# Kernel tuning notes

Measured on AMD Instinct MI355X. Metric: run time of the kernel, lower is better.

Reference implementation:

```python
import jax, jax.numpy as jnp
import numpy as np
from jax import lax

D = 768
C = 37          # num_classes + 1
PAD_ID = C - 1  # label_init puts '[PAD]' last
B, S = 128, 512


def setup_inputs() -> dict:
    key = jax.random.key(0)
    ks = jax.random.split(key, 8)
    x = jax.random.normal(ks[0], (B, S, D), dtype=jnp.float32)
    W = jax.random.normal(ks[1], (D, C), dtype=jnp.float32) * (1.0 / np.sqrt(D))
    b = jnp.zeros((C,), dtype=jnp.float32)
    start = jax.random.uniform(ks[2], (C,), minval=-0.1, maxval=0.1)
    end = jax.random.uniform(ks[3], (C,), minval=-0.1, maxval=0.1)
    trans = jax.random.uniform(ks[4], (C, C), minval=-0.1, maxval=0.1)
    labels = jax.random.randint(ks[5], (B, S), 0, C)
    lengths = jax.random.randint(ks[6], (B,), 16, S + 1)
    mask = (jnp.arange(S)[None, :] < lengths[:, None])  # first column always True
    return {"x": x, "W": W, "b": b, "start": start, "end": end,
            "trans": trans, "labels": labels, "mask": mask}


def _crf(emissions, labels, mask, start, end, trans):
    # time-major, as in pytorch-crf
    em = jnp.transpose(emissions, (1, 0, 2))      # [S, B, C]
    tg = labels.T                                  # [S, B]
    mkb = mask.T                                   # [S, B] bool
    mkf = mkb.astype(em.dtype)
    bidx = jnp.arange(em.shape[1])

    # ---- gold path score ----
    score0 = start[tg[0]] + em[0, bidx, tg[0]]
    def step_score(carry, inp):
        prev_tag, s = carry
        e_t, t_t, mf, mb = inp
        s = s + (trans[prev_tag, t_t] + e_t[bidx, t_t]) * mf
        prev_tag = jnp.where(mb, t_t, prev_tag)
        return (prev_tag, s), None
    (last_tag, score), _ = lax.scan(step_score, (tg[0], score0),
                                    (em[1:], tg[1:], mkf[1:], mkb[1:]))
    score = score + end[last_tag]

    # ---- log partition (forward algorithm) ----
    alpha0 = start[None, :] + em[0]               # [B, C]
    def step_norm(alpha, inp):
        e_t, mb = inp
        nxt = jax.nn.logsumexp(alpha[:, :, None] + trans[None, :, :], axis=1) + e_t
        return jnp.where(mb[:, None], nxt, alpha), None
    alpha, _ = lax.scan(step_norm, alpha0, (em[1:], mkb[1:]))
    logZ = jax.nn.logsumexp(alpha + end[None, :], axis=1)
    ll = jnp.sum(score - logZ)                    # reduction='sum'

    # ---- Viterbi decode ----
    ident = jnp.arange(C)[None, :]
    v0 = start[None, :] + em[0]
    def step_vit(v, inp):
        e_t, mb = inp
        cand = v[:, :, None] + trans[None, :, :]  # [B, prev, cur]
        bp = jnp.argmax(cand, axis=1)             # [B, C]
        nxt = jnp.max(cand, axis=1) + e_t
        v = jnp.where(mb[:, None], nxt, v)
        bp = jnp.where(mb[:, None], bp, ident)    # identity at padded steps
        return v, bp
    v, bps = lax.scan(step_vit, v0, (em[1:], mkb[1:]))  # bps: [S-1, B, C]
    last = jnp.argmax(v + end[None, :], axis=1)   # [B]
    def back(tag, bp):
        return bp[bidx, tag], tag
    first, rest = lax.scan(back, last, bps, reverse=True)
    tags = jnp.concatenate([first[None, :], rest], axis=0).T  # [B, S]
    tags = jnp.where(mask, tags, PAD_ID)
    return ll, tags


def reference(x, W, b, start, end, trans, labels, mask):
    emissions = jnp.einsum('bsd,dc->bsc', x, W) + b  # linear head
    log_likelihood, tags = _crf(emissions, labels, mask, start, end, trans)
    return log_likelihood, tags
```

## Files before the change

### kernel.cpp

```cpp
#include <hip/hip_runtime.h>

#define Bq 128
#define Sq 512
#define Cq 37
#define Dq 768
#define VST 40

typedef __attribute__((ext_vector_type(2))) float f32x2;
typedef __attribute__((ext_vector_type(4))) float f32x4;
typedef __attribute__((ext_vector_type(8))) short bf16x8;

static __device__ __forceinline__ f32x2 pk_fma(f32x2 a, f32x2 b, f32x2 c) {
  f32x2 d; asm("v_pk_fma_f32 %0, %1, %2, %3" : "=v"(d) : "v"(a), "v"(b), "v"(c));
  return d;
}
static __device__ __forceinline__ f32x2 pk_add(f32x2 a, f32x2 b) {
  f32x2 d; asm("v_pk_add_f32 %0, %1, %2" : "=v"(d) : "v"(a), "v"(b));
  return d;
}
static __device__ __forceinline__ float bcast(float v, int p) {
  return __int_as_float(__builtin_amdgcn_ds_bpermute(p << 2, __float_as_int(v)));
}

#define REP18(X) X(0)X(1)X(2)X(3)X(4)X(5)X(6)X(7)X(8)X(9)X(10)X(11)X(12)X(13) \
  X(14)X(15)X(16)X(17)
#define REP37(X) X(0)X(1)X(2)X(3)X(4)X(5)X(6)X(7)X(8)X(9)X(10)X(11)X(12)X(13) \
  X(14)X(15)X(16)X(17)X(18)X(19)X(20)X(21)X(22)X(23)X(24)X(25)X(26)X(27)X(28) \
  X(29)X(30)X(31)X(32)X(33)X(34)X(35)X(36)

__global__ __launch_bounds__(256) void prep_kernel(
    const float* __restrict__ W, unsigned short* __restrict__ Wbh,
    unsigned short* __restrict__ Wbl)
{
  int i = blockIdx.x * 256 + threadIdx.x;
  if (i >= 24 * 3 * 64 * 8) return;
  int ks = i / 1536, rem = i % 1536;
  int nt = rem / 512, rem2 = rem % 512;
  int lane = rem2 >> 3, j = rem2 & 7;
  int k = ks * 32 + (lane >> 4) * 8 + j;
  int c = nt * 16 + (lane & 15);
  float w = (c < Cq) ? W[(size_t)k * Cq + c] : 0.f;
  unsigned u = __float_as_uint(w);
  unsigned short h = (unsigned short)(u >> 16);
  float hr = __uint_as_float((unsigned)h << 16);
  float r = w - hr;
  Wbh[i] = h;
  Wbl[i] = (unsigned short)(__float_as_uint(r) >> 16);
}

__global__ __launch_bounds__(256) void emis_kernel(
    const float* __restrict__ x, const unsigned short* __restrict__ Wbh,
    const unsigned short* __restrict__ Wbl, const float* __restrict__ bias,
    float* __restrict__ em)
{
  int tid = threadIdx.x, lane = tid & 63;
  int wv = tid >> 6;
  int tokBase = blockIdx.x * 64 + wv * 16;
  int row = lane & 15, kg = lane >> 4;
  const float* xr = x + (size_t)(tokBase + row) * Dq + kg * 8;
  const bf16x8* Bh = (const bf16x8*)Wbh;
  const bf16x8* Bl = (const bf16x8*)Wbl;
  f32x4 acc0 = {0.f, 0.f, 0.f, 0.f};
  f32x4 acc1 = {0.f, 0.f, 0.f, 0.f};
  f32x4 acc2 = {0.f, 0.f, 0.f, 0.f};

  float4 c0 = *(const float4*)(xr);
  float4 c1 = *(const float4*)(xr + 4);
  for (int ks = 0; ks < 24; ++ks) {
    float4 n0, n1;
    if (ks < 23) {
      n0 = *(const float4*)(xr + (ks + 1) * 32);
      n1 = *(const float4*)(xr + (ks + 1) * 32 + 4);
    }
    bf16x8 ah, al;
#define SPLIT(J, V) { unsigned u = __float_as_uint(V); \
    unsigned short h = (unsigned short)(u >> 16); \
    float hr = __uint_as_float((unsigned)h << 16); \
    float rr = (V) - hr; \
    ah[J] = (short)h; al[J] = (short)(__float_as_uint(rr) >> 16); }
    SPLIT(0, c0.x) SPLIT(1, c0.y) SPLIT(2, c0.z) SPLIT(3, c0.w)
    SPLIT(4, c1.x) SPLIT(5, c1.y) SPLIT(6, c1.z) SPLIT(7, c1.w)
#undef SPLIT
    int fi = (ks * 3) * 64 + lane;
    bf16x8 bh0 = Bh[fi], bh1 = Bh[fi + 64], bh2 = Bh[fi + 128];
    bf16x8 bl0 = Bl[fi], bl1 = Bl[fi + 64], bl2 = Bl[fi + 128];
    acc0 = __builtin_amdgcn_mfma_f32_16x16x32_bf16(al, bh0, acc0, 0, 0, 0);
    acc1 = __builtin_amdgcn_mfma_f32_16x16x32_bf16(al, bh1, acc1, 0, 0, 0);
    acc2 = __builtin_amdgcn_mfma_f32_16x16x32_bf16(al, bh2, acc2, 0, 0, 0);
    acc0 = __builtin_amdgcn_mfma_f32_16x16x32_bf16(ah, bl0, acc0, 0, 0, 0);
    acc1 = __builtin_amdgcn_mfma_f32_16x16x32_bf16(ah, bl1, acc1, 0, 0, 0);
    acc2 = __builtin_amdgcn_mfma_f32_16x16x32_bf16(ah, bl2, acc2, 0, 0, 0);
    acc0 = __builtin_amdgcn_mfma_f32_16x16x32_bf16(ah, bh0, acc0, 0, 0, 0);
    acc1 = __builtin_amdgcn_mfma_f32_16x16x32_bf16(ah, bh1, acc1, 0, 0, 0);
    acc2 = __builtin_amdgcn_mfma_f32_16x16x32_bf16(ah, bh2, acc2, 0, 0, 0);
    c0 = n0; c1 = n1;
  }
  int colc = lane & 15;
#pragma unroll
  for (int r = 0; r < 4; ++r) {
    size_t tok = (size_t)tokBase + kg * 4 + r;
    em[tok * Cq + colc]      = acc0[r] + bias[colc];
    em[tok * Cq + 16 + colc] = acc1[r] + bias[16 + colc];
    if (colc < 5)
      em[tok * Cq + 32 + colc] = acc2[r] + bias[32 + colc];
  }
}

__global__ __launch_bounds__(320) void crf_serial_kernel(
    const float* __restrict__ em, const float* __restrict__ startv,
    const float* __restrict__ endv, const float* __restrict__ trans,
    const int* __restrict__ labels, const unsigned char* __restrict__ maskb,
    float* __restrict__ vhist, float* __restrict__ llp,
    int* __restrict__ lenp, int* __restrict__ lastp, int* __restrict__ midp)
{
  __shared__ float semm[(Sq + 4) * Cq];
  __shared__ __align__(16) float sxA[64];
  __shared__ __align__(16) float sxB[64];
  __shared__ __align__(16) float sxC[64];
  __shared__ __align__(16) float sxD[64];
  __shared__ float mrgA[64], mrgB[64], mrgV[64], mrgU[64];
  __shared__ float s_score;
  int b = blockIdx.x;
  int tid = threadIdx.x, wid = tid >> 6, lane = tid & 63;
  int cl = lane < Cq ? lane : Cq - 1;

  int esz4 = (maskb[1] == 0) ? 1 : 0;
  int len = 0;
#pragma unroll
  for (int k = 0; k < 8; ++k) {
    size_t t = (size_t)lane + (size_t)k * 64;
    unsigned char mb = esz4 ? maskb[((size_t)b * Sq + t) * 4] : maskb[(size_t)b * Sq + t];
    len += (mb != 0);
  }
#pragma unroll
  for (int off = 32; off; off >>= 1) len += __shfl_xor(len, off);
  int m = len >> 1;

  const float4* src4 = (const float4*)(em + (size_t)b * Sq * Cq);
  float4* dst4 = (float4*)semm;
  for (int i = tid; i < (Sq * Cq) / 4; i += 320) dst4[i] = src4[i];
  if (tid < 4 * Cq) semm[Sq * Cq + tid] = 0.f;
  __syncthreads();

  const float L2E = 1.4426950408889634f, LN2 = 0.6931471805599453f;

  if (wid == 0) {
    f32x2 E2[18];
#pragma unroll
    for (int i = 0; i < 18; ++i) {
      E2[i][0] = exp2f(trans[(2 * i) * Cq + cl] * L2E);
      E2[i][1] = exp2f(trans[(2 * i + 1) * Cq + cl] * L2E);
    }
    float E36 = exp2f(trans[36 * Cq + cl] * L2E);
    const float4* se4 = (const float4*)sxA;
    float a0 = (lane < Cq) ? (startv[cl] + semm[cl]) : -3.0e38f;
    float K0 = bcast(a0, 0);
    float ez = (lane < Cq) ? exp2f((a0 - K0) * L2E) : 0.f;
    int eacc = 0;
    float wA = exp2f(semm[1 * Cq + cl] * L2E), wB = exp2f(semm[2 * Cq + cl] * L2E);
    float wC = exp2f(semm[3 * Cq + cl] * L2E), wD = exp2f(semm[4 * Cq + cl] * L2E);
    for (int t = 1; t <= m; ++t) {
      sxA[lane] = ez;
      int tn = (t + 4 <= m) ? t + 4 : m;
      float raw = semm[tn * Cq + cl];
      float4 gv[10];
#pragma unroll
      for (int q = 0; q < 10; ++q) gv[q] = se4[q];
      int e0 = ((__float_as_int(gv[0].x) >> 23) & 255) - 127;
      float scale = __int_as_float((127 - e0) << 23);
      f32x2 sa = {0.f, 0.f}, sb2 = {0.f, 0.f};
#define FPK(i) { f32x2 g; \
      g[0] = ((i) & 1) ? gv[(i) >> 1].z : gv[(i) >> 1].x; \
      g[1] = ((i) & 1) ? gv[(i) >> 1].w : gv[(i) >> 1].y; \
      if ((i) & 1) sb2 = pk_fma(g, E2[i], sb2); else sa = pk_fma(g, E2[i], sa); }
      REP18(FPK)
#undef FPK
      float dot = ((sa[0] + sb2[0]) + (sa[1] + sb2[1])) + gv[9].x * E36;
      float wcur = wA; wA = wB; wB = wC; wC = wD;
      ez = dot * (wcur * scale);
      eacc += e0;
      wD = exp2f(raw * L2E);
    }
    mrgA[lane] = (lane < Cq) ? LN2 * (log2f(ez) + (float)eacc) + K0 : -3.0e38f;
  } else if (wid == 1) {
    f32x2 E2[18];
#pragma unroll
    for (int i = 0; i < 18; ++i) {
      E2[i][0] = exp2f(trans[cl * Cq + 2 * i] * L2E);
      E2[i][1] = exp2f(trans[cl * Cq + 2 * i + 1] * L2E);
    }
    float E36 = exp2f(trans[cl * Cq + 36] * L2E);
    const float4* se4 = (const float4*)sxB;
    float b0v = (lane < Cq) ? endv[cl] : -3.0e38f;
    float KB = bcast(b0v, 0);
    float bz = (lane < Cq) ? exp2f((b0v - KB) * L2E) : 0.f;
    int eacc = 0;
    float wA = exp2f(semm[(len - 1) * Cq + cl] * L2E);
    float wB = exp2f(semm[(len - 2) * Cq + cl] * L2E);
    float wC = exp2f(semm[(len - 3) * Cq + cl] * L2E);
    float wD = exp2f(semm[(len - 4) * Cq + cl] * L2E);
    for (int t = len - 2; t >= m; --t) {
      float wcur = wA; wA = wB; wB = wC; wC = wD;
      float s = bz * wcur;
      sxB[lane] = s;
      int tn = (t - 3 > 0) ? t - 3 : 0;
      float raw = semm[tn * Cq + cl];
      float4 gv[10];
#pragma unroll
      for (int q = 0; q < 10; ++q) gv[q] = se4[q];
      int e0 = ((__float_as_int(gv[0].x) >> 23) & 255) - 127;
      float scale = __int_as_float((127 - e0) << 23);
      f32x2 sa = {0.f, 0.f}, sb2 = {0.f, 0.f};
#define FPK(i) { f32x2 g; \
      g[0] = ((i) & 1) ? gv[(i) >> 1].z : gv[(i) >> 1].x; \
      g[1] = ((i) & 1) ? gv[(i) >> 1].w : gv[(i) >> 1].y; \
      if ((i) & 1) sb2 = pk_fma(g, E2[i], sb2); else sa = pk_fma(g, E2[i], sa); }
      REP18(FPK)
#undef FPK
      float dot = ((sa[0] + sb2[0]) + (sa[1] + sb2[1])) + gv[9].x * E36;
      bz = dot * scale;
      eacc += e0;
      wD = exp2f(raw * L2E);
    }
    mrgB[lane] = (lane < Cq) ? LN2 * (log2f(bz) + (float)eacc) + KB : -3.0e38f;
  } else if (wid == 2) {
    f32x2 T2[18];
#pragma unroll
    for (int i = 0; i < 18; ++i) {
      T2[i][0] = trans[(2 * i) * Cq + cl];
      T2[i][1] = trans[(2 * i + 1) * Cq + cl];
    }
    float T36 = trans[36 * Cq + cl];
    const float4* sv4 = (const float4*)sxC;
    float v = (lane < Cq) ? (startv[cl] + semm[cl]) : -3.0e38f;
    if (lane < Cq) vhist[((size_t)b * Sq) * VST + cl] = v;
    float emA = semm[1 * Cq + cl], emB = semm[2 * Cq + cl];
    float emC = semm[3 * Cq + cl], emD = semm[4 * Cq + cl];
    for (int t = 1; t <= m; ++t) {
      sxC[lane] = v;
      int tn = (t + 4 <= m) ? t + 4 : m;
      float raw = semm[tn * Cq + cl];
      float4 gv[10];
#pragma unroll
      for (int q = 0; q < 10; ++q) gv[q] = sv4[q];
      float m0 = -3.0e38f, m1 = -3.0e38f, m2 = -3.0e38f, m3 = -3.0e38f;
#define VPK(i) { f32x2 g; \
      g[0] = ((i) & 1) ? gv[(i) >> 1].z : gv[(i) >> 1].x; \
      g[1] = ((i) & 1) ? gv[(i) >> 1].w : gv[(i) >> 1].y; \
      f32x2 c = pk_add(g, T2[i]); \
      if (((i) & 3) == 0) m0 = fmaxf(fmaxf(m0, c[0]), c[1]); \
      else if (((i) & 3) == 1) m1 = fmaxf(fmaxf(m1, c[0]), c[1]); \
      else if (((i) & 3) == 2) m2 = fmaxf(fmaxf(m2, c[0]), c[1]); \
      else m3 = fmaxf(fmaxf(m3, c[0]), c[1]); }
      REP18(VPK)
#undef VPK
      float c36 = gv[9].x + T36;
      float best = fmaxf(fmaxf(fmaxf(m0, m1), fmaxf(m2, m3)), c36);
      float emc = emA; emA = emB; emB = emC; emC = emD;
      v = (lane < Cq) ? best + emc : -3.0e38f;
      if (lane < Cq) vhist[((size_t)b * Sq + t) * VST + cl] = v;
      emD = raw;
    }
    mrgV[lane] = v;
  } else if (wid == 3) {
    f32x2 T2[18];
#pragma unroll
    for (int i = 0; i < 18; ++i) {
      T2[i][0] = trans[cl * Cq + 2 * i];
      T2[i][1] = trans[cl * Cq + 2 * i + 1];
    }
    float T36 = trans[cl * Cq + 36];
    const float4* sv4 = (const float4*)sxD;
    float u = (lane < Cq) ? endv[cl] : -3.0e38f;
    if (lane < Cq) vhist[((size_t)b * Sq + (len - 1)) * VST + cl] = u;
    float emA = semm[(len - 1) * Cq + cl], emB = semm[(len - 2) * Cq + cl];
    float emC = semm[(len - 3) * Cq + cl], emD = semm[(len - 4) * Cq + cl];
    for (int t = len - 2; t >= m; --t) {
      float emc = emA; emA = emB; emB = emC; emC = emD;
      float s = u + emc;
      sxD[lane] = s;
      int tn = (t - 3 > 0) ? t - 3 : 0;
      float raw = semm[tn * Cq + cl];
      float4 gv[10];
#pragma unroll
      for (int q = 0; q < 10; ++q) gv[q] = sv4[q];
      float m0 = -3.0e38f, m1 = -3.0e38f, m2 = -3.0e38f, m3 = -3.0e38f;
#define VPK(i) { f32x2 g; \
      g[0] = ((i) & 1) ? gv[(i) >> 1].z : gv[(i) >> 1].x; \
      g[1] = ((i) & 1) ? gv[(i) >> 1].w : gv[(i) >> 1].y; \
      f32x2 c = pk_add(g, T2[i]); \
      if (((i) & 3) == 0) m0 = fmaxf(fmaxf(m0, c[0]), c[1]); \
      else if (((i) & 3) == 1) m1 = fmaxf(fmaxf(m1, c[0]), c[1]); \
      else if (((i) & 3) == 2) m2 = fmaxf(fmaxf(m2, c[0]), c[1]); \
      else m3 = fmaxf(fmaxf(m3, c[0]), c[1]); }
      REP18(VPK)
#undef VPK
      float c36 = gv[9].x + T36;
      float best = fmaxf(fmaxf(fmaxf(m0, m1), fmaxf(m2, m3)), c36);
      u = (lane < Cq) ? best : -3.0e38f;
      if (lane < Cq && t > m) vhist[((size_t)b * Sq + t) * VST + cl] = u;
      emD = raw;
    }
    mrgU[lane] = u;
  } else {
    const int* lab = labels + (size_t)b * Sq;
    float sc = 0.f;
#pragma unroll
    for (int k = 0; k < 8; ++k) {
      int t = 1 + lane + k * 64;
      if (t < len) {
        int lp = lab[t - 1], lt = lab[t];
        sc += trans[lp * Cq + lt] + semm[t * Cq + lt];
      }
    }
#pragma unroll
    for (int off = 32; off; off >>= 1) sc += __shfl_xor(sc, off);
    if (lane == 0) {
      int l0 = lab[0], lf = lab[len - 1];
      s_score = sc + startv[l0] + semm[l0] + endv[lf];
    }
  }
  __syncthreads();
  if (wid == 0) {
    float xv = (lane < Cq) ? mrgA[lane] + mrgB[lane] : -3.0e38f;
    float mm = xv;
#pragma unroll
    for (int off = 32; off; off >>= 1) mm = fmaxf(mm, __shfl_xor(mm, off));
    float es = exp2f((xv - mm) * L2E);
#pragma unroll
    for (int off = 32; off; off >>= 1) es += __shfl_xor(es, off);
    float logZ = mm + log2f(es) * LN2;
    float pv = (lane < Cq) ? mrgV[lane] + mrgU[lane] : -3.0e38f;
    int idx = (lane < Cq) ? lane : 1000;
#pragma unroll
    for (int off = 32; off; off >>= 1) {
      float po = __shfl_xor(pv, off); int io = __shfl_xor(idx, off);
      if (po > pv || (po == pv && io < idx)) { pv = po; idx = io; }
    }
    if (lane == 0) {
      llp[b] = s_score - logZ;
      lastp[b] = idx; lenp[b] = len; midp[b] = m;
    }
  }
}

__global__ __launch_bounds__(256) void crf_bp_kernel(
    const float* __restrict__ vhist, const float* __restrict__ em,
    const float* __restrict__ trans, const int* __restrict__ lenp,
    const int* __restrict__ midp, unsigned char* __restrict__ bp)
{
  int role = blockIdx.x >> 9;
  int bid = blockIdx.x & 511;
  int b = bid >> 2, chunk = bid & 3;
  int wid = threadIdx.x >> 6, lane = threadIdx.x & 63;
  int cl = lane < Cq ? lane : Cq - 1;
  int len = lenp[b], m = midp[b];
  int rl9 = lane < VST ? lane : VST - 1;
  if (role == 0) {
#define DECLT(i) float T##i = trans[(i) * Cq + cl];
    REP37(DECLT)
#undef DECLT
    int tend = 1 + (chunk + 1) * 128; if (tend > m + 1) tend = m + 1;
    for (int t = 1 + chunk * 128 + wid; t < tend; t += 4) {
      float vr = vhist[((size_t)b * Sq + (t - 1)) * VST + rl9];
#define BCASTB(i) float br##i = bcast(vr, (i));
      REP37(BCASTB)
#undef BCASTB
      float best = -3.0e38f; int bi = 0;
#define BARG(i) { float cnd = br##i + T##i; if (cnd > best) { best = cnd; bi = (i); } }
      REP37(BARG)
#undef BARG
      if (lane < Cq) bp[((size_t)b * VST + cl) * Sq + t] = (unsigned char)bi;
    }
  } else {
#define DECLR(i) float R##i = trans[cl * Cq + (i)];
    REP37(DECLR)
#undef DECLR
    int er = lane < Cq ? lane : 0;
    int s0 = m + 1 + chunk * 128 + wid;
    int send = m + 1 + (chunk + 1) * 128; if (send > len) send = len;
    for (int s = s0; s < send; s += 4) {
      float uv = vhist[((size_t)b * Sq + s) * VST + rl9];
      float ev = em[((size_t)b * Sq + s) * Cq + er];
      float sv = uv + ev;
#define BCASTB(i) float br##i = bcast(sv, (i));
      REP37(BCASTB)
#undef BCASTB
      float best = -3.0e38f; int bi = 0;
#define BARG(i) { float cnd = br##i + R##i; if (cnd > best) { best = cnd; bi = (i); } }
      REP37(BARG)
#undef BARG
      if (lane < Cq) bp[((size_t)b * VST + cl) * Sq + s] = (unsigned char)bi;
    }
  }
}

__global__ __launch_bounds__(64) void crf_back_kernel(
    const unsigned char* __restrict__ bp, const int* __restrict__ lenp,
    const int* __restrict__ lastp, const int* __restrict__ midp,
    float* __restrict__ outp)
{
  int b = blockIdx.x, lane = threadIdx.x;
  int len = __builtin_amdgcn_readfirstlane(lenp[b]);
  int m = __builtin_amdgcn_readfirstlane(midp[b]);
  int cstar = __builtin_amdgcn_readfirstlane(lastp[b]);
  int row = lane < VST ? lane : VST - 1;
  const uint4* src = (const uint4*)(bp + ((size_t)b * VST + row) * Sq);
  unsigned r[128];
#pragma unroll
  for (int k = 0; k < 32; ++k) {
    uint4 q = src[k];
    r[4 * k] = q.x; r[4 * k + 1] = q.y; r[4 * k + 2] = q.z; r[4 * k + 3] = q.w;
  }
  unsigned vt[8];
#pragma unroll
  for (int j = 0; j < 8; ++j) vt[j] = 0u;
#pragma unroll
  for (int j = 0; j < 8; ++j)
    vt[j] = (lane == (m & 63) && (m >> 6) == j) ? (unsigned)cstar : vt[j];
  {
    int tag = cstar;
#pragma unroll
    for (int t = 1; t <= 510; ++t) {
      int word = __builtin_amdgcn_readlane((int)r[t >> 2], tag);
      int nt = (word >> ((t & 3) * 8)) & 0xff;
      bool live = (t > m) && (t < len);
      tag = live ? nt : tag;
      vt[t >> 6] = (lane == (t & 63) && live) ? (unsigned)tag : vt[t >> 6];
    }
  }
  {
    int tag = cstar;
#pragma unroll
    for (int t = 510; t >= 0; --t) {
      int word = __builtin_amdgcn_readlane((int)r[(t + 1) >> 2], tag);
      int nt = (word >> (((t + 1) & 3) * 8)) & 0xff;
      bool live = (t + 1 <= m);
      tag = live ? nt : tag;
      vt[t >> 6] = (lane == (t & 63) && live) ? (unsigned)tag : vt[t >> 6];
    }
  }
#pragma unroll
  for (int j = 0; j < 8; ++j) {
    int t = j * 64 + lane;
    float o = (t < len) ? (float)(int)vt[j] : 36.0f;
    outp[(size_t)b * Sq + t] = o;
  }
}

__global__ __launch_bounds__(64) void ll_reduce_kernel(
    const float* __restrict__ llp, float* __restrict__ outp)
{
  int lane = threadIdx.x;
  float s = llp[lane] + llp[lane + 64];
#pragma unroll
  for (int off = 32; off; off >>= 1) s += __shfl_xor(s, off);
  if (lane == 0) outp[0] = s;
}

extern "C" void kernel_launch(void* const* d_in, const int* in_sizes, int n_in,
                              void* d_out, int out_size, void* d_ws, size_t ws_size,
                              hipStream_t stream)
{
  const float* x      = (const float*)d_in[0];
  const float* W      = (const float*)d_in[1];
  const float* bias   = (const float*)d_in[2];
  const float* startv = (const float*)d_in[3];
  const float* endv   = (const float*)d_in[4];
  const float* trans  = (const float*)d_in[5];
  const int*   labels = (const int*)d_in[6];
  const unsigned char* maskb = (const unsigned char*)d_in[7];
  float* out = (float*)d_out;

  char* ws = (char*)d_ws;
  float* em            = (float*)(ws);
  float* vhist         = (float*)(ws + 9699328);
  unsigned char* bpbuf = (unsigned char*)(ws + 20185088);
  float* llp           = (float*)(ws + 22806528);
  int*   lenp          = (int*)(ws + 22807552);
  int*   lastp         = (int*)(ws + 22808064);
  int*   midp          = (int*)(ws + 22809088);
  unsigned short* Wbh  = (unsigned short*)(ws + 22809600);
  unsigned short* Wbl  = (unsigned short*)(ws + 22883328);

  prep_kernel<<<144, 256, 0, stream>>>(W, Wbh, Wbl);
  emis_kernel<<<1024, 256, 0, stream>>>(x, Wbh, Wbl, bias, em);
  crf_serial_kernel<<<128, 320, 0, stream>>>(em, startv, endv, trans, labels, maskb,
                                             vhist, llp, lenp, lastp, midp);
  crf_bp_kernel<<<1024, 256, 0, stream>>>(vhist, em, trans, lenp, midp, bpbuf);
  crf_back_kernel<<<128, 64, 0, stream>>>(bpbuf, lenp, lastp, midp, out + 1);
  ll_reduce_kernel<<<1, 64, 0, stream>>>(llp, out);
}
```

Baseline: 203.6 us.

## Fuse serial CRF, backpointer and backtrace kernels into one LDS-resident kernel

The forward/backward Viterbi score history now stays in shared memory instead of global memory. The same block then computes backpointers and runs the backtrace, which removes two kernel launches and the global round trip of the score history and backpointers. The emission buffer in shared memory is reused to hold the backpointers. In exchange, backpointer computation runs on only 128 blocks of 4 waves instead of 1024 blocks, and the kernel's shared-memory use now comes close to the per-CU limit, which leaves room for only one block per CU.

After: 187.3 us. -8.0%, faster.

```diff
diff --git a/kernel.cpp b/kernel.cpp
--- a/kernel.cpp
+++ b/kernel.cpp
@@ -4,7 +4,6 @@
 #define Sq 512
 #define Cq 37
 #define Dq 768
-#define VST 40
 
 typedef __attribute__((ext_vector_type(2))) float f32x2;
 typedef __attribute__((ext_vector_type(4))) float f32x4;
@@ -106,20 +105,21 @@
   }
 }
 
-__global__ __launch_bounds__(320) void crf_serial_kernel(
+__global__ __launch_bounds__(320) void crf_mega_kernel(
     const float* __restrict__ em, const float* __restrict__ startv,
     const float* __restrict__ endv, const float* __restrict__ trans,
     const int* __restrict__ labels, const unsigned char* __restrict__ maskb,
-    float* __restrict__ vhist, float* __restrict__ llp,
-    int* __restrict__ lenp, int* __restrict__ lastp, int* __restrict__ midp)
+    float* __restrict__ llp, float* __restrict__ outp)
 {
   __shared__ float semm[(Sq + 4) * Cq];
+  __shared__ float vh[Sq * 40];
   __shared__ __align__(16) float sxA[64];
   __shared__ __align__(16) float sxB[64];
   __shared__ __align__(16) float sxC[64];
   __shared__ __align__(16) float sxD[64];
   __shared__ float mrgA[64], mrgB[64], mrgV[64], mrgU[64];
   __shared__ float s_score;
+  __shared__ int s_cstar;
   int b = blockIdx.x;
   int tid = threadIdx.x, wid = tid >> 6, lane = tid & 63;
   int cl = lane < Cq ? lane : Cq - 1;
@@ -233,7 +233,7 @@
     float T36 = trans[36 * Cq + cl];
     const float4* sv4 = (const float4*)sxC;
     float v = (lane < Cq) ? (startv[cl] + semm[cl]) : -3.0e38f;
-    if (lane < Cq) vhist[((size_t)b * Sq) * VST + cl] = v;
+    vh[0 * 40 + lane] = (lane < Cq) ? v : -3.0e38f;
     float emA = semm[1 * Cq + cl], emB = semm[2 * Cq + cl];
     float emC = semm[3 * Cq + cl], emD = semm[4 * Cq + cl];
     for (int t = 1; t <= m; ++t) {
@@ -258,7 +258,7 @@
       float best = fmaxf(fmaxf(fmaxf(m0, m1), fmaxf(m2, m3)), c36);
       float emc = emA; emA = emB; emB = emC; emC = emD;
       v = (lane < Cq) ? best + emc : -3.0e38f;
-      if (lane < Cq) vhist[((size_t)b * Sq + t) * VST + cl] = v;
+      vh[t * 40 + lane] = v;
       emD = raw;
     }
     mrgV[lane] = v;
@@ -272,13 +272,13 @@
     float T36 = trans[cl * Cq + 36];
     const float4* sv4 = (const float4*)sxD;
     float u = (lane < Cq) ? endv[cl] : -3.0e38f;
-    if (lane < Cq) vhist[((size_t)b * Sq + (len - 1)) * VST + cl] = u;
     float emA = semm[(len - 1) * Cq + cl], emB = semm[(len - 2) * Cq + cl];
     float emC = semm[(len - 3) * Cq + cl], emD = semm[(len - 4) * Cq + cl];
     for (int t = len - 2; t >= m; --t) {
       float emc = emA; emA = emB; emB = emC; emC = emD;
       float s = u + emc;
       sxD[lane] = s;
+      vh[(t + 1) * 40 + lane] = (lane < Cq) ? s : -3.0e38f;
       int tn = (t - 3 > 0) ? t - 3 : 0;
       float raw = semm[tn * Cq + cl];
       float4 gv[10];
@@ -298,7 +298,6 @@
       float c36 = gv[9].x + T36;
       float best = fmaxf(fmaxf(fmaxf(m0, m1), fmaxf(m2, m3)), c36);
       u = (lane < Cq) ? best : -3.0e38f;
-      if (lane < Cq && t > m) vhist[((size_t)b * Sq + t) * VST + cl] = u;
       emD = raw;
     }
     mrgU[lane] = u;
@@ -321,6 +320,8 @@
     }
   }
   __syncthreads();
+
+  unsigned char* bpl = (unsigned char*)semm;
   if (wid == 0) {
     float xv = (lane < Cq) ? mrgA[lane] + mrgB[lane] : -3.0e38f;
     float mm = xv;
@@ -337,114 +338,89 @@
       float po = __shfl_xor(pv, off); int io = __shfl_xor(idx, off);
       if (po > pv || (po == pv && io < idx)) { pv = po; idx = io; }
     }
-    if (lane == 0) {
-      llp[b] = s_score - logZ;
-      lastp[b] = idx; lenp[b] = len; midp[b] = m;
-    }
-  }
-}
-
-__global__ __launch_bounds__(256) void crf_bp_kernel(
-    const float* __restrict__ vhist, const float* __restrict__ em,
-    const float* __restrict__ trans, const int* __restrict__ lenp,
-    const int* __restrict__ midp, unsigned char* __restrict__ bp)
-{
-  int role = blockIdx.x >> 9;
-  int bid = blockIdx.x & 511;
-  int b = bid >> 2, chunk = bid & 3;
-  int wid = threadIdx.x >> 6, lane = threadIdx.x & 63;
-  int cl = lane < Cq ? lane : Cq - 1;
-  int len = lenp[b], m = midp[b];
-  int rl9 = lane < VST ? lane : VST - 1;
-  if (role == 0) {
+    if (lane == 0) { llp[b] = s_score - logZ; s_cstar = idx; }
+  } else if (wid <= 2) {
 #define DECLT(i) float T##i = trans[(i) * Cq + cl];
     REP37(DECLT)
 #undef DECLT
-    int tend = 1 + (chunk + 1) * 128; if (tend > m + 1) tend = m + 1;
-    for (int t = 1 + chunk * 128 + wid; t < tend; t += 4) {
-      float vr = vhist[((size_t)b * Sq + (t - 1)) * VST + rl9];
-#define BCASTB(i) float br##i = bcast(vr, (i));
-      REP37(BCASTB)
-#undef BCASTB
+    for (int t = wid; t <= m; t += 2) {
+      const float4* vr4 = (const float4*)&vh[(t - 1) * 40];
+      float4 gv[10];
+#pragma unroll
+      for (int q = 0; q < 10; ++q) gv[q] = vr4[q];
+      float br[40]; float4* br4 = (float4*)br;
+#pragma unroll
+      for (int q = 0; q < 10; ++q) br4[q] = gv[q];
       float best = -3.0e38f; int bi = 0;
-#define BARG(i) { float cnd = br##i + T##i; if (cnd > best) { best = cnd; bi = (i); } }
+#define BARG(i) { float cnd = br[i] + T##i; if (cnd > best) { best = cnd; bi = (i); } }
       REP37(BARG)
 #undef BARG
-      if (lane < Cq) bp[((size_t)b * VST + cl) * Sq + t] = (unsigned char)bi;
+      if (lane < Cq) bpl[cl * 520 + t] = (unsigned char)bi;
     }
   } else {
 #define DECLR(i) float R##i = trans[cl * Cq + (i)];
     REP37(DECLR)
 #undef DECLR
-    int er = lane < Cq ? lane : 0;
-    int s0 = m + 1 + chunk * 128 + wid;
-    int send = m + 1 + (chunk + 1) * 128; if (send > len) send = len;
-    for (int s = s0; s < send; s += 4) {
-      float uv = vhist[((size_t)b * Sq + s) * VST + rl9];
-      float ev = em[((size_t)b * Sq + s) * Cq + er];
-      float sv = uv + ev;
-#define BCASTB(i) float br##i = bcast(sv, (i));
-      REP37(BCASTB)
-#undef BCASTB
+    for (int s = m + 1 + (wid - 3); s < len; s += 2) {
+      const float4* vr4 = (const float4*)&vh[s * 40];
+      float4 gv[10];
+#pragma unroll
+      for (int q = 0; q < 10; ++q) gv[q] = vr4[q];
+      float br[40]; float4* br4 = (float4*)br;
+#pragma unroll
+      for (int q = 0; q < 10; ++q) br4[q] = gv[q];
       float best = -3.0e38f; int bi = 0;
-#define BARG(i) { float cnd = br##i + R##i; if (cnd > best) { best = cnd; bi = (i); } }
+#define BARG(i) { float cnd = br[i] + R##i; if (cnd > best) { best = cnd; bi = (i); } }
       REP37(BARG)
 #undef BARG
-      if (lane < Cq) bp[((size_t)b * VST + cl) * Sq + s] = (unsigned char)bi;
-    }
-  }
-}
-
-__global__ __launch_bounds__(64) void crf_back_kernel(
-    const unsigned char* __restrict__ bp, const int* __restrict__ lenp,
-    const int* __restrict__ lastp, const int* __restrict__ midp,
-    float* __restrict__ outp)
-{
-  int b = blockIdx.x, lane = threadIdx.x;
-  int len = __builtin_amdgcn_readfirstlane(lenp[b]);
-  int m = __builtin_amdgcn_readfirstlane(midp[b]);
-  int cstar = __builtin_amdgcn_readfirstlane(lastp[b]);
-  int row = lane < VST ? lane : VST - 1;
-  const uint4* src = (const uint4*)(bp + ((size_t)b * VST + row) * Sq);
-  unsigned r[128];
-#pragma unroll
-  for (int k = 0; k < 32; ++k) {
-    uint4 q = src[k];
-    r[4 * k] = q.x; r[4 * k + 1] = q.y; r[4 * k + 2] = q.z; r[4 * k + 3] = q.w;
-  }
-  unsigned vt[8];
-#pragma unroll
-  for (int j = 0; j < 8; ++j) vt[j] = 0u;
-#pragma unroll
-  for (int j = 0; j < 8; ++j)
-    vt[j] = (lane == (m & 63) && (m >> 6) == j) ? (unsigned)cstar : vt[j];
-  {
-    int tag = cstar;
-#pragma unroll
-    for (int t = 1; t <= 510; ++t) {
-      int word = __builtin_amdgcn_readlane((int)r[t >> 2], tag);
-      int nt = (word >> ((t & 3) * 8)) & 0xff;
-      bool live = (t > m) && (t < len);
-      tag = live ? nt : tag;
-      vt[t >> 6] = (lane == (t & 63) && live) ? (unsigned)tag : vt[t >> 6];
-    }
-  }
-  {
-    int tag = cstar;
-#pragma unroll
-    for (int t = 510; t >= 0; --t) {
-      int word = __builtin_amdgcn_readlane((int)r[(t + 1) >> 2], tag);
-      int nt = (word >> (((t + 1) & 3) * 8)) & 0xff;
-      bool live = (t + 1 <= m);
-      tag = live ? nt : tag;
-      vt[t >> 6] = (lane == (t & 63) && live) ? (unsigned)tag : vt[t >> 6];
-    }
-  }
-#pragma unroll
-  for (int j = 0; j < 8; ++j) {
-    int t = j * 64 + lane;
-    float o = (t < len) ? (float)(int)vt[j] : 36.0f;
-    outp[(size_t)b * Sq + t] = o;
+      if (lane < Cq) bpl[cl * 520 + s] = (unsigned char)bi;
+    }
+  }
+  __syncthreads();
+
+  if (wid == 0) {
+    int cstar = __builtin_amdgcn_readfirstlane(s_cstar);
+    int lenv = __builtin_amdgcn_readfirstlane(len);
+    int mv = __builtin_amdgcn_readfirstlane(m);
+    int rowc = lane < Cq ? lane : Cq - 1;
+    const unsigned* rw = (const unsigned*)(bpl + rowc * 520);
+    unsigned r[128];
+#pragma unroll
+    for (int k = 0; k < 128; ++k) r[k] = rw[k];
+    unsigned vt[8];
+#pragma unroll
+    for (int j = 0; j < 8; ++j) vt[j] = 0u;
+#pragma unroll
+    for (int j = 0; j < 8; ++j)
+      vt[j] = (lane == (mv & 63) && (mv >> 6) == j) ? (unsigned)cstar : vt[j];
+    {
+      int tag = cstar;
+#pragma unroll
+      for (int t = 1; t <= 510; ++t) {
+        int word = __builtin_amdgcn_readlane((int)r[t >> 2], tag);
+        int nt = (word >> ((t & 3) * 8)) & 0xff;
+        bool live = (t > mv) && (t < lenv);
+        tag = live ? nt : tag;
+        vt[t >> 6] = (lane == (t & 63) && live) ? (unsigned)tag : vt[t >> 6];
+      }
+    }
+    {
+      int tag = cstar;
+#pragma unroll
+      for (int t = 510; t >= 0; --t) {
+        int word = __builtin_amdgcn_readlane((int)r[(t + 1) >> 2], tag);
+        int nt = (word >> (((t + 1) & 3) * 8)) & 0xff;
+        bool live = (t + 1 <= mv);
+        tag = live ? nt : tag;
+        vt[t >> 6] = (lane == (t & 63) && live) ? (unsigned)tag : vt[t >> 6];
+      }
+    }
+#pragma unroll
+    for (int j = 0; j < 8; ++j) {
+      int t = j * 64 + lane;
+      float o = (t < lenv) ? (float)(int)vt[j] : 36.0f;
+      outp[(size_t)b * Sq + t] = o;
+    }
   }
 }
 
@@ -474,20 +450,13 @@
 
   char* ws = (char*)d_ws;
   float* em            = (float*)(ws);
-  float* vhist         = (float*)(ws + 9699328);
-  unsigned char* bpbuf = (unsigned char*)(ws + 20185088);
-  float* llp           = (float*)(ws + 22806528);
-  int*   lenp          = (int*)(ws + 22807552);
-  int*   lastp         = (int*)(ws + 22808064);
-  int*   midp          = (int*)(ws + 22809088);
-  unsigned short* Wbh  = (unsigned short*)(ws + 22809600);
-  unsigned short* Wbl  = (unsigned short*)(ws + 22883328);
+  float* llp           = (float*)(ws + 9699328);
+  unsigned short* Wbh  = (unsigned short*)(ws + 9699840);
+  unsigned short* Wbl  = (unsigned short*)(ws + 9773568);
 
   prep_kernel<<<144, 256, 0, stream>>>(W, Wbh, Wbl);
   emis_kernel<<<1024, 256, 0, stream>>>(x, Wbh, Wbl, bias, em);
-  crf_serial_kernel<<<128, 320, 0, stream>>>(em, startv, endv, trans, labels, maskb,
-                                             vhist, llp, lenp, lastp, midp);
-  crf_bp_kernel<<<1024, 256, 0, stream>>>(vhist, em, trans, lenp, midp, bpbuf);
-  crf_back_kernel<<<128, 64, 0, stream>>>(bpbuf, lenp, lastp, midp, out + 1);
+  crf_mega_kernel<<<128, 320, 0, stream>>>(em, startv, endv, trans, labels, maskb,
+                                           llp, out + 1);
   ll_reduce_kernel<<<1, 64, 0, stream>>>(llp, out);
 }
```
